# Kernel tuning notes

Measured on AMD Instinct MI355X. Metric: run time of the kernel, lower is better.

## Reference

```python
import jax, jax.numpy as jnp
import numpy as np

HIDDEN = 1000
IN_DIM = 1024


def setup_inputs() -> dict:
    key = jax.random.key(0)
    ks = jax.random.split(key, 9)
    s = 0.05
    return {
        "x": jax.random.normal(ks[0], (64, 128, IN_DIM), dtype=jnp.float32),
        "W1": jax.random.normal(ks[1], (IN_DIM, 4 * HIDDEN), dtype=jnp.float32) * s,
        "U1": jax.random.normal(ks[2], (HIDDEN, 4 * HIDDEN), dtype=jnp.float32) * s,
        "b1": jnp.zeros((4 * HIDDEN,), dtype=jnp.float32),
        "W2": jax.random.normal(ks[3], (HIDDEN, 4 * HIDDEN), dtype=jnp.float32) * s,
        "U2": jax.random.normal(ks[4], (HIDDEN, 4 * HIDDEN), dtype=jnp.float32) * s,
        "b2": jnp.zeros((4 * HIDDEN,), dtype=jnp.float32),
        "Wo": jax.random.normal(ks[5], (HIDDEN, 6), dtype=jnp.float32) * s,
        "bo": jnp.zeros((6,), dtype=jnp.float32),
    }


def _lstm_step(h, c, z):
    # Keras LSTMCell gate order: i, f, g(cell), o
    i, f, g, o = jnp.split(z, 4, axis=-1)
    i = jax.nn.sigmoid(i)
    f = jax.nn.sigmoid(f)
    o = jax.nn.sigmoid(o)
    c_new = f * c + i * jnp.tanh(g)
    h_new = o * jnp.tanh(c_new)
    return h_new, c_new


def reference(x, W1, U1, b1, W2, U2, b2, Wo, bo):
    B = x.shape[0]
    xs = jnp.swapaxes(x, 0, 1)  # [T, B, D]

    def step(carry, xt):
        h1, c1, h2, c2 = carry
        z1 = xt @ W1 + h1 @ U1 + b1
        h1, c1 = _lstm_step(h1, c1, z1)
        z2 = h1 @ W2 + h2 @ U2 + b2
        h2, c2 = _lstm_step(h2, c2, z2)
        return (h1, c1, h2, c2), None

    zeros = jnp.zeros((B, HIDDEN), dtype=x.dtype)
    (h1, c1, h2, c2), _ = jax.lax.scan(step, (zeros, zeros, zeros, zeros), xs)
    # RNN(return_sequences=False) returns last top-cell hidden state
    return h2 @ Wo + bo
```

## Files before the change

### kernel.cpp

```cpp
#include <hip/hip_runtime.h>
#include <hip/hip_bf16.h>

#define TT 128
#define DD 1024
#define HH 1000
#define NBLK 252
#define RING 16

typedef float f32x4 __attribute__((ext_vector_type(4)));
typedef __bf16 bf16x8 __attribute__((ext_vector_type(8)));

__device__ __forceinline__ bf16x8 asbf(f32x4 v) { return __builtin_bit_cast(bf16x8, v); }

__device__ __forceinline__ void ld_a(bf16x8* d, const char* p) {
    asm volatile("global_load_dwordx4 %0, %1, off sc0" : "=v"(*d) : "v"(p));
}
__device__ __forceinline__ void st_h32(char* p, unsigned v) {
    asm volatile("global_store_dword %0, %1, off sc0 sc1" :: "v"(p), "v"(v) : "memory");
}
__device__ __forceinline__ void st_ctl(unsigned* p, unsigned v) {
    asm volatile("global_store_dword %0, %1, off sc0 sc1" :: "v"(p), "v"(v) : "memory");
}

#define AT_RLX __ATOMIC_RELAXED
#define SC_AGT __HIP_MEMORY_SCOPE_AGENT

__global__ void zero_ws(unsigned int* __restrict__ p, int nwords) {
    int i = blockIdx.x * blockDim.x + threadIdx.x;
    if (i < nwords) p[i] = 0u;
}

__global__ void cast_x(const float* __restrict__ x, __bf16* __restrict__ xfh) {
    int gid = blockIdx.x * 256 + threadIdx.x;
    int lane = gid & 63;
    int mt = (gid >> 6) & 3;
    int ks = (gid >> 8) & 31;
    int t  = gid >> 13;
    int row = mt * 16 + (lane & 15);
    int k0  = ks * 32 + (lane >> 4) * 8;
    const float* sp = x + ((size_t)row * TT + t) * 1024 + k0;
    float4 v0 = *(const float4*)sp;
    float4 v1 = *(const float4*)(sp + 4);
    float f[8] = {v0.x, v0.y, v0.z, v0.w, v1.x, v1.y, v1.z, v1.w};
    bf16x8 hv;
#pragma unroll
    for (int j = 0; j < 8; ++j) hv[j] = (__bf16)f[j];
    ((bf16x8*)xfh)[gid] = hv;
}

__global__ __launch_bounds__(256) void pack_w2(
    const float* __restrict__ W1, const float* __restrict__ U1,
    const float* __restrict__ W2, const float* __restrict__ U2,
    __bf16* __restrict__ w1h, __bf16* __restrict__ w2h)
{
    int nt = blockIdx.x;
    int layer = blockIdx.y;
    const float* R1 = layer ? W2 : W1;
    const float* R2 = layer ? U2 : U1;
    int k1v = layer ? HH : 1024;
    __bf16* dh = layer ? w2h : w1h;
    int tid = threadIdx.x;

    __shared__ float lt[64][21];

    int kk = tid >> 2, g = tid & 3;
    for (int c = 0; c < 32; ++c) {
        int k = c * 64 + kk;
        float4 v = {0.f, 0.f, 0.f, 0.f};
        if (k < 1024) {
            if (k < k1v) v = *(const float4*)(R1 + (size_t)k * 4000 + g * 1000 + nt * 4);
        } else {
            int k2 = k - 1024;
            if (k2 < HH) v = *(const float4*)(R2 + (size_t)k2 * 4000 + g * 1000 + nt * 4);
        }
        lt[kk][g * 4 + 0] = v.x; lt[kk][g * 4 + 1] = v.y;
        lt[kk][g * 4 + 2] = v.z; lt[kk][g * 4 + 3] = v.w;
        __syncthreads();
        if (tid < 128) {
            int kbl = tid >> 4, col = tid & 15;
            int li = (col & 3) * 4 + (col >> 2);
            bf16x8 hv;
#pragma unroll
            for (int j = 0; j < 8; ++j) hv[j] = (__bf16)lt[kbl * 8 + j][li];
            size_t unit = ((size_t)nt * 256 + c * 8 + kbl) * 16 + col;
            ((bf16x8*)dh)[unit] = hv;
        }
        __syncthreads();
    }
}

__global__ __launch_bounds__(256, 1) void lstm_persist(
    const __bf16* __restrict__ xfh,
    const __bf16* __restrict__ w1h, const __bf16* __restrict__ w2h,
    const float* __restrict__ b1, const float* __restrict__ b2,
    __bf16* hbuf, unsigned int* ctrl)
{
    unsigned* xcdm    = ctrl + 32;
    unsigned* xcdFlag = ctrl + 384;
    unsigned* arr     = ctrl + 512;

    const int bid = blockIdx.x;
    const int layer = bid >= 126;
    const int r0 = layer ? bid - 126 : bid;
    const int bh = r0 >= 63;
    const int nb = bh ? r0 - 63 : r0;
    const int tid = threadIdx.x;
    const int lane = tid & 63, w = tid >> 6;
    const int op = w >> 1, kh = w & 1;
    const int ln = lane & 15, kg = lane >> 4;

    const char* h1ring = (const char*)hbuf;
    const char* h2ring = (const char*)(hbuf + (size_t)RING * 65536);

    __shared__ unsigned s_ldr;
    if (tid == 0) {
        unsigned x;
        asm volatile("s_getreg_b32 %0, hwreg(HW_REG_XCC_ID)" : "=s"(x));
        x &= 7u;
        unsigned old = __hip_atomic_fetch_add(&xcdm[x], 1u, AT_RLX, SC_AGT);
        s_ldr = (x << 8) | (old == 0u ? 1u : 0u);
    }

    const f32x4* wfh = (const f32x4*)(layer ? w2h : w1h);
    f32x4 WH[64];
#pragma unroll
    for (int tl = 0; tl < 4; ++tl) {
        int nt = nb * 4 + tl; if (nt > 249) nt = 249;
#pragma unroll
        for (int ks = 0; ks < 16; ++ks) {
            int kb = op * 128 + kh * 64 + ks * 4 + kg;
            WH[tl * 16 + ks] = wfh[((size_t)nt * 256 + kb) * 16 + ln];
        }
    }
#define PIN8(p0,p1,p2,p3,p4,p5,p6,p7) \
    asm volatile("" : "+a"(p0),"+a"(p1),"+a"(p2),"+a"(p3),"+a"(p4),"+a"(p5),"+a"(p6),"+a"(p7))
    PIN8(WH[0],WH[1],WH[2],WH[3],WH[4],WH[5],WH[6],WH[7]);
    PIN8(WH[8],WH[9],WH[10],WH[11],WH[12],WH[13],WH[14],WH[15]);
    PIN8(WH[16],WH[17],WH[18],WH[19],WH[20],WH[21],WH[22],WH[23]);
    PIN8(WH[24],WH[25],WH[26],WH[27],WH[28],WH[29],WH[30],WH[31]);
    PIN8(WH[32],WH[33],WH[34],WH[35],WH[36],WH[37],WH[38],WH[39]);
    PIN8(WH[40],WH[41],WH[42],WH[43],WH[44],WH[45],WH[46],WH[47]);
    PIN8(WH[48],WH[49],WH[50],WH[51],WH[52],WH[53],WH[54],WH[55]);
    PIN8(WH[56],WH[57],WH[58],WH[59],WH[60],WH[61],WH[62],WH[63]);
#undef PIN8

    const float* bias = layer ? b2 : b1;
    const int gb = tid >> 3;
    const int gcl0 = (tid * 2) & 15;
    float bias_q[2][4];
#pragma unroll
    for (int q = 0; q < 2; ++q) {
        int n = nb * 16 + gcl0 + q; if (n > HH - 1) n = HH - 1;
#pragma unroll
        for (int g = 0; g < 4; ++g) bias_q[q][g] = bias[(size_t)g * HH + n];
    }
    float creg[2] = {0.f, 0.f};

    __shared__ float zs[4][32][68];
    __syncthreads();

#pragma unroll 1
    for (int t = 0; t <= TT; ++t) {
        const bool active = layer ? (t >= 1) : (t <= TT - 1);
        if (active) {
            const char *pAh;
            char *poh;
            if (layer == 0) {
                if (op == 0) pAh = (const char*)xfh + (size_t)t * 131072;
                else         pAh = h1ring + (size_t)((t - 1) & (RING - 1)) * 131072;
                poh = (char*)(h1ring + (size_t)(t & (RING - 1)) * 131072);
            } else {
                if (op == 0) pAh = h1ring + (size_t)((t - 1) & (RING - 1)) * 131072;
                else         pAh = h2ring + (size_t)((t - 2) & (RING - 1)) * 131072;
                poh = (char*)(h2ring + (size_t)((t - 1) & (RING - 1)) * 131072);
            }
            pAh += ((size_t)kh * 4096 + bh * 128 + lane) * 16;

            f32x4 acc[4][2];
#pragma unroll
            for (int tl = 0; tl < 4; ++tl)
#pragma unroll
                for (int mt = 0; mt < 2; ++mt) acc[tl][mt] = (f32x4){0.f, 0.f, 0.f, 0.f};

            bf16x8 rh[8][2];
#define LDB(s, k) do { _Pragma("unroll") \
    for (int mt = 0; mt < 2; ++mt) \
        ld_a(&rh[s][mt], pAh + (size_t)((k) * 256 + mt * 64) * 16); \
    } while (0)
#define CPK(k, s) do { _Pragma("unroll") \
    for (int tl = 0; tl < 4; ++tl) { \
        bf16x8 wh_ = asbf(WH[tl * 16 + (k)]); \
        _Pragma("unroll") \
        for (int mt = 0; mt < 2; ++mt) \
            acc[tl][mt] = __builtin_amdgcn_mfma_f32_16x16x32_bf16(rh[s][mt], wh_, acc[tl][mt], 0, 0, 0); \
    } } while (0)

            LDB(0, 0); LDB(1, 1); LDB(2, 2); LDB(3, 3);
            LDB(4, 4); LDB(5, 5); LDB(6, 6); LDB(7, 7);
#pragma unroll
            for (int ks = 0; ks < 16; ++ks) {
                if (ks <= 8)       asm volatile("s_waitcnt vmcnt(14)" ::: "memory");
                else if (ks == 9)  asm volatile("s_waitcnt vmcnt(12)" ::: "memory");
                else if (ks == 10) asm volatile("s_waitcnt vmcnt(10)" ::: "memory");
                else if (ks == 11) asm volatile("s_waitcnt vmcnt(8)"  ::: "memory");
                else if (ks == 12) asm volatile("s_waitcnt vmcnt(6)"  ::: "memory");
                else if (ks == 13) asm volatile("s_waitcnt vmcnt(4)"  ::: "memory");
                else if (ks == 14) asm volatile("s_waitcnt vmcnt(2)"  ::: "memory");
                else               asm volatile("s_waitcnt vmcnt(0)"  ::: "memory");
                __builtin_amdgcn_sched_barrier(0);
                CPK(ks, ks & 7);
                if (ks < 8) LDB(ks & 7, ks + 8);
            }
#undef LDB
#undef CPK

#pragma unroll
            for (int tl = 0; tl < 4; ++tl)
#pragma unroll
                for (int mt = 0; mt < 2; ++mt)
#pragma unroll
                    for (int r = 0; r < 4; ++r)
                        zs[w][mt * 16 + kg * 4 + r][tl * 16 + ln] = acc[tl][mt][r];
            __syncthreads();

            {
                int cc = (gcl0 >> 2) * 16 + (gcl0 & 3) * 4;
                float hv2[2];
#pragma unroll
                for (int q = 0; q < 2; ++q) {
                    float zg[4];
#pragma unroll
                    for (int g = 0; g < 4; ++g)
                        zg[g] = zs[0][gb][cc + q * 4 + g] + zs[1][gb][cc + q * 4 + g]
                              + zs[2][gb][cc + q * 4 + g] + zs[3][gb][cc + q * 4 + g]
                              + bias_q[q][g];
                    float ig = 1.f / (1.f + __expf(-zg[0]));
                    float fg = 1.f / (1.f + __expf(-zg[1]));
                    float gg = 1.f - 2.f / (__expf(2.f * zg[2]) + 1.f);
                    float og = 1.f / (1.f + __expf(-zg[3]));
                    float cn = fg * creg[q] + ig * gg;
                    creg[q] = cn;
                    hv2[q] = og * (1.f - 2.f / (__expf(2.f * cn) + 1.f));
                }
                if (nb * 16 + gcl0 < HH) {
                    unsigned pk = (unsigned)__builtin_bit_cast(unsigned short, (__bf16)hv2[0])
                                | ((unsigned)__builtin_bit_cast(unsigned short, (__bf16)hv2[1]) << 16);
                    int mt_l = gb >> 4, lnn = gb & 15;
                    int kgsel = gcl0 >> 3, j0 = gcl0 & 7;
                    size_t unit = (((size_t)(nb >> 1) * 4 + bh * 2 + mt_l) * 64)
                                + ((nb & 1) * 2 + kgsel) * 16 + lnn;
                    st_h32(poh + unit * 16 + (size_t)j0 * 2, pk);
                }
            }
            asm volatile("s_waitcnt vmcnt(0)" ::: "memory");
        }

        if (t < TT) {
            __syncthreads();
            const unsigned tp1 = (unsigned)(t + 1);
            if (w == 0) {
                if (tid == 0) st_ctl(arr + (size_t)bid * 4, tp1);
                const unsigned* a0 = arr + (size_t)lane * 4;
                bool done = false;
                while (!done) {
                    unsigned v0, v1, v2, v3;
                    asm volatile("global_load_dword %0, %1, off sc0 sc1" : "=v"(v0) : "v"(a0));
                    asm volatile("global_load_dword %0, %1, off sc0 sc1" : "=v"(v1) : "v"(a0 + 256));
                    asm volatile("global_load_dword %0, %1, off sc0 sc1" : "=v"(v2) : "v"(a0 + 512));
                    asm volatile("global_load_dword %0, %1, off sc0 sc1" : "=v"(v3) : "v"(a0 + 768));
                    asm volatile("s_waitcnt vmcnt(0)" ::: "memory");
                    bool ok = (v0 >= tp1) && (v1 >= tp1) && (v2 >= tp1)
                           && ((lane + 192 >= NBLK) || (v3 >= tp1));
                    done = __all(ok);
                    if (!done) __builtin_amdgcn_s_sleep(1);
                }
                if ((tp1 & (RING - 1u)) == 0u) {
                    if (tid == 0) {
                        unsigned info = s_ldr;
                        unsigned* fP = xcdFlag + (info >> 8) * 16;
                        if (info & 1u) {
                            __builtin_amdgcn_fence(__ATOMIC_ACQUIRE, "agent");
                            asm volatile("s_waitcnt vmcnt(0) lgkmcnt(0)" ::: "memory");
                            __hip_atomic_store(fP, tp1, AT_RLX, SC_AGT);
                        } else {
                            while (__hip_atomic_load(fP, AT_RLX, SC_AGT) < tp1)
                                __builtin_amdgcn_s_sleep(1);
                        }
                    }
                    __builtin_amdgcn_wave_barrier();
                }
            }
            __syncthreads();
        }
    }
}

__global__ void out_proj(const __bf16* __restrict__ h2h,
                         const float* __restrict__ Wo, const float* __restrict__ bo,
                         float* __restrict__ out)
{
    int b = blockIdx.x, tid = threadIdx.x;
    int mt = b >> 4, ln = b & 15;
    float acc[6] = {0, 0, 0, 0, 0, 0};
    for (int n = tid; n < HH; n += 256) {
        int ks = n >> 5, kg = (n >> 3) & 3, j = n & 7;
        size_t idx = (((size_t)ks * 4 + mt) * 64 + kg * 16 + ln) * 8 + j;
        float h = (float)h2h[idx];
#pragma unroll
        for (int o = 0; o < 6; ++o) acc[o] += h * Wo[n * 6 + o];
    }
#pragma unroll
    for (int o = 0; o < 6; ++o)
        for (int off = 32; off; off >>= 1) acc[o] += __shfl_down(acc[o], off, 64);
    __shared__ float red[4][6];
    int lane = tid & 63, wv = tid >> 6;
    if (lane == 0) {
#pragma unroll
        for (int o = 0; o < 6; ++o) red[wv][o] = acc[o];
    }
    __syncthreads();
    if (tid < 6) {
        float s = bo[tid];
#pragma unroll
        for (int w = 0; w < 4; ++w) s += red[w][tid];
        out[b * 6 + tid] = s;
    }
}

extern "C" void kernel_launch(void* const* d_in, const int* in_sizes, int n_in,
                              void* d_out, int out_size, void* d_ws, size_t ws_size,
                              hipStream_t stream) {
    const float* x  = (const float*)d_in[0];
    const float* W1 = (const float*)d_in[1];
    const float* U1 = (const float*)d_in[2];
    const float* b1 = (const float*)d_in[3];
    const float* W2 = (const float*)d_in[4];
    const float* U2 = (const float*)d_in[5];
    const float* b2 = (const float*)d_in[6];
    const float* Wo = (const float*)d_in[7];
    const float* bo = (const float*)d_in[8];
    float* out = (float*)d_out;

    char* p = (char*)d_ws;
    __bf16* hbuf = (__bf16*)p; p += (size_t)2 * RING * 65536 * 2;
    unsigned int* ctrl = (unsigned int*)p; p += 8192;
    __bf16* xfh = (__bf16*)p; p += (size_t)8388608 * 2;
    __bf16* w1h = (__bf16*)p; p += (size_t)8192000 * 2;
    __bf16* w2h = (__bf16*)p; p += (size_t)8192000 * 2;

    zero_ws<<<4104, 256, 0, stream>>>((unsigned int*)d_ws, 1050624);
    cast_x<<<4096, 256, 0, stream>>>(x, xfh);
    pack_w2<<<dim3(250, 2), 256, 0, stream>>>(W1, U1, W2, U2, w1h, w2h);

    lstm_persist<<<NBLK, 256, 0, stream>>>(xfh, w1h, w2h, b1, b2, hbuf, ctrl);

    out_proj<<<64, 256, 0, stream>>>(hbuf + (size_t)(RING + 15) * 65536, Wo, bo, out);
}
```

Baseline: 718.9 us.

## Zero only needed workspace slices and repack weights by k-block rows

The workspace zeroing kernel now clears only three selected regions (two ring slots of the h buffer and the control area) instead of the whole 4 MB prefix. The weight packing kernel is reorganized so each block loads 8 full contiguous rows of W/U into shared memory and emits all N-tiles for that k-block, replacing strided per-tile column reads. This aims to cut setup memory traffic and improve coalescing of the fp32 weight reads. The risk is correctness if lstm_persist relies on other zero-initialized ring slots, and the larger shared-memory footprint lowers occupancy of the pack kernel.

```diff
diff --git a/kernel.cpp b/kernel.cpp
--- a/kernel.cpp
+++ b/kernel.cpp
@@ -25,9 +25,14 @@
 #define AT_RLX __ATOMIC_RELAXED
 #define SC_AGT __HIP_MEMORY_SCOPE_AGENT
 
-__global__ void zero_ws(unsigned int* __restrict__ p, int nwords) {
-    int i = blockIdx.x * blockDim.x + threadIdx.x;
-    if (i < nwords) p[i] = 0u;
+__global__ void zero_sel(char* __restrict__ ws) {
+    int i = blockIdx.x * 256 + threadIdx.x;
+    if (i >= 67584) return;
+    unsigned* p;
+    if (i < 32768)      p = (unsigned*)(ws + (size_t)15 * 131072) + i;
+    else if (i < 65536) p = (unsigned*)(ws + (size_t)31 * 131072) + (i - 32768);
+    else                p = (unsigned*)(ws + (size_t)32 * 131072) + (i - 65536);
+    *p = 0u;
 }
 
 __global__ void cast_x(const float* __restrict__ x, __bf16* __restrict__ xfh) {
@@ -48,12 +53,12 @@
     ((bf16x8*)xfh)[gid] = hv;
 }
 
-__global__ __launch_bounds__(256) void pack_w2(
+__global__ __launch_bounds__(256) void pack_w3(
     const float* __restrict__ W1, const float* __restrict__ U1,
     const float* __restrict__ W2, const float* __restrict__ U2,
     __bf16* __restrict__ w1h, __bf16* __restrict__ w2h)
 {
-    int nt = blockIdx.x;
+    int kb = blockIdx.x;
     int layer = blockIdx.y;
     const float* R1 = layer ? W2 : W1;
     const float* R2 = layer ? U2 : U1;
@@ -61,31 +66,33 @@
     __bf16* dh = layer ? w2h : w1h;
     int tid = threadIdx.x;
 
-    __shared__ float lt[64][21];
-
-    int kk = tid >> 2, g = tid & 3;
-    for (int c = 0; c < 32; ++c) {
-        int k = c * 64 + kk;
-        float4 v = {0.f, 0.f, 0.f, 0.f};
-        if (k < 1024) {
-            if (k < k1v) v = *(const float4*)(R1 + (size_t)k * 4000 + g * 1000 + nt * 4);
-        } else {
-            int k2 = k - 1024;
-            if (k2 < HH) v = *(const float4*)(R2 + (size_t)k2 * 4000 + g * 1000 + nt * 4);
+    const float* src = (kb < 128) ? R1 : R2;
+    const int kmax = (kb < 128) ? k1v : HH;
+    const int base = (kb & 127) * 8;
+
+    __shared__ float lt[8][4008];
+
+#pragma unroll 1
+    for (int r = 0; r < 8; ++r) {
+        bool valid = (base + r) < kmax;
+        const float* rp = src + (size_t)(base + r) * 4000;
+        for (int c4 = tid; c4 < 1000; c4 += 256) {
+            float4 v = valid ? *(const float4*)(rp + c4 * 4)
+                             : (float4){0.f, 0.f, 0.f, 0.f};
+            lt[r][c4 * 4 + 0] = v.x; lt[r][c4 * 4 + 1] = v.y;
+            lt[r][c4 * 4 + 2] = v.z; lt[r][c4 * 4 + 3] = v.w;
         }
-        lt[kk][g * 4 + 0] = v.x; lt[kk][g * 4 + 1] = v.y;
-        lt[kk][g * 4 + 2] = v.z; lt[kk][g * 4 + 3] = v.w;
-        __syncthreads();
-        if (tid < 128) {
-            int kbl = tid >> 4, col = tid & 15;
-            int li = (col & 3) * 4 + (col >> 2);
-            bf16x8 hv;
-#pragma unroll
-            for (int j = 0; j < 8; ++j) hv[j] = (__bf16)lt[kbl * 8 + j][li];
-            size_t unit = ((size_t)nt * 256 + c * 8 + kbl) * 16 + col;
-            ((bf16x8*)dh)[unit] = hv;
-        }
-        __syncthreads();
+    }
+    __syncthreads();
+
+    for (int u = tid; u < 4000; u += 256) {
+        int nt = u >> 4, col = u & 15;
+        int scol = (col & 3) * 1000 + nt * 4 + (col >> 2);
+        bf16x8 hv;
+#pragma unroll
+        for (int j = 0; j < 8; ++j) hv[j] = (__bf16)lt[j][scol];
+        size_t unit = ((size_t)nt * 256 + kb) * 16 + col;
+        ((bf16x8*)dh)[unit] = hv;
     }
 }
 
@@ -348,9 +355,9 @@
     __bf16* w1h = (__bf16*)p; p += (size_t)8192000 * 2;
     __bf16* w2h = (__bf16*)p; p += (size_t)8192000 * 2;
 
-    zero_ws<<<4104, 256, 0, stream>>>((unsigned int*)d_ws, 1050624);
+    zero_sel<<<264, 256, 0, stream>>>((char*)d_ws);
     cast_x<<<4096, 256, 0, stream>>>(x, xfh);
-    pack_w2<<<dim3(250, 2), 256, 0, stream>>>(W1, U1, W2, U2, w1h, w2h);
+    pack_w3<<<dim3(256, 2), 256, 0, stream>>>(W1, U1, W2, U2, w1h, w2h);
 
     lstm_persist<<<NBLK, 256, 0, stream>>>(xfh, w1h, w2h, b1, b2, hbuf, ctrl);
 
```

Result: faster. 665.8 us, median of 2 (-7.4%).
